# Performance work log

Measured on AMD Instinct MI355X. Metric: run time of the kernel, lower is better.

Reference implementation:

```python
import jax, jax.numpy as jnp
import numpy as np

EPS = 1e-5  # flax BatchNorm default epsilon


def setup_inputs() -> dict:
    key = jax.random.key(0)
    ks = jax.random.split(key, 4)
    E, D, H = 6400000, 12, 12
    N = 100000
    return {
        "edges": jax.random.normal(ks[0], (E, D), dtype=jnp.float32),
        "bn_scale": jnp.ones((D,), jnp.float32),
        "bn_bias": jnp.zeros((D,), jnp.float32),
        "bn_mean": jnp.zeros((D,), jnp.float32),
        "bn_var": jnp.ones((D,), jnp.float32),
        "W1": jax.random.normal(ks[1], (D, H), dtype=jnp.float32) / np.sqrt(D),
        "b1": jnp.zeros((H,), jnp.float32),
        "W2": jax.random.normal(ks[2], (H, H), dtype=jnp.float32) / np.sqrt(H),
        "b2": jnp.zeros((H,), jnp.float32),
        "receivers": jax.random.randint(ks[3], (E,), 0, N, dtype=jnp.int32),
        "num_nodes": N,
    }


def reference(edges, bn_scale, bn_bias, bn_mean, bn_var, W1, b1, W2, b2, receivers, num_nodes):
    # EdgeEncoder (eval mode): BatchNorm(running stats) -> Dense(12) -> ReLU -> Dense(12)
    x = (edges - bn_mean) * (bn_scale * jax.lax.rsqrt(bn_var + EPS)) + bn_bias
    x = jax.nn.relu(x @ W1 + b1)
    x = x @ W2 + b2  # [E, 12] per-edge messages
    # aggregate messages into receiver nodes (update_node_fn returns this directly)
    nodes = jax.ops.segment_sum(x, receivers, num_segments=num_nodes)  # [N, 12]
    return nodes
```

## Files before the change

### kernel.cpp

```cpp
#include <hip/hip_runtime.h>

#define D      12
#define ASTR   13
#define LOGNPB 7
#define NPB    128
#define CAPBF  5120
#define CAPF   9216
#define EPB    16384
#define ABLK   256
#define SBLK   256
#define CBLK   256
#define SPLIT  2

#define SWZ(p) ((p) ^ (((p) >> 5) & 31))

static __device__ __forceinline__ unsigned f2bf(float f) {
    union { float f; unsigned u; } v; v.f = f;
    unsigned r = v.u + 0x7FFFu + ((v.u >> 16) & 1u);
    return r >> 16;
}
static __device__ __forceinline__ float bf_lo(unsigned u) {
    union { unsigned u; float f; } v; v.u = u << 16; return v.f;
}
static __device__ __forceinline__ float bf_hi(unsigned u) {
    union { unsigned u; float f; } v; v.u = u & 0xFFFF0000u; return v.f;
}

__global__ __launch_bounds__(256) void cvt_bf16(
    const float* __restrict__ in, unsigned* __restrict__ outw,
    long n8 , long ntot )
{
    long i = (long)blockIdx.x * 256 + threadIdx.x;
    const long stride = (long)gridDim.x * 256;
    for (; i < n8; i += stride) {
        const float4* p = reinterpret_cast<const float4*>(in + i * 8);
        float4 a = p[0], b = p[1];
        uint4 w;
        w.x = f2bf(a.x) | (f2bf(a.y) << 16);
        w.y = f2bf(a.z) | (f2bf(a.w) << 16);
        w.z = f2bf(b.x) | (f2bf(b.y) << 16);
        w.w = f2bf(b.z) | (f2bf(b.w) << 16);
        reinterpret_cast<uint4*>(outw)[i] = w;
    }
    if (blockIdx.x == 0 && threadIdx.x == 0) {
        for (long j = n8 * 8; j < ntot; ++j)
            reinterpret_cast<unsigned short*>(outw)[j] = (unsigned short)f2bf(in[j]);
    }
}

__global__ __launch_bounds__(ABLK) void passA_hist(
    const int* __restrict__ receivers, long E, int nbuck,
    int* __restrict__ cnt )
{
    extern __shared__ int hist[];
    for (int i = threadIdx.x; i < nbuck; i += ABLK) hist[i] = 0;
    __syncthreads();
    long e0 = (long)blockIdx.x * EPB;
    long e1 = e0 + EPB; if (e1 > E) e1 = E;
    for (long e = e0 + threadIdx.x; e < e1; e += ABLK) {
        int r = receivers[e];
        atomicAdd(&hist[r >> LOGNPB], 1);
    }
    __syncthreads();
    int* row = cnt + (long)blockIdx.x * nbuck;
    for (int i = threadIdx.x; i < nbuck; i += ABLK) row[i] = hist[i];
}

__global__ __launch_bounds__(SBLK) void passS1_colscan(
    int* __restrict__ cnt, int nblk, int nbuck, int* __restrict__ totals)
{
    int b = blockIdx.x;
    int t = threadIdx.x;
    __shared__ int csum[SBLK];
    int per = (nblk + SBLK - 1) / SBLK;
    int i0 = t * per;
    int i1 = i0 + per; if (i1 > nblk) i1 = nblk;
    int s = 0;
    for (int i = i0; i < i1; ++i) s += cnt[(long)i * nbuck + b];
    csum[t] = s;
    __syncthreads();
    for (int off = 1; off < SBLK; off <<= 1) {
        int add = (t >= off) ? csum[t - off] : 0;
        __syncthreads();
        csum[t] += add;
        __syncthreads();
    }
    int run = csum[t] - s;
    for (int i = i0; i < i1; ++i) {
        long a = (long)i * nbuck + b;
        int tmp = cnt[a];
        cnt[a] = run;
        run += tmp;
    }
    if (t == SBLK - 1) totals[b] = csum[SBLK - 1];
}

__global__ __launch_bounds__(1024) void passS2_basescan(
    const int* __restrict__ totals, int* __restrict__ base, int nbuck)
{
    __shared__ int sh[1024];
    int t = threadIdx.x;
    int v = (t < nbuck) ? totals[t] : 0;
    sh[t] = v;
    __syncthreads();
    for (int off = 1; off < 1024; off <<= 1) {
        int add = (t >= off) ? sh[t - off] : 0;
        __syncthreads();
        sh[t] += add;
        __syncthreads();
    }
    if (t < nbuck) base[t] = sh[t] - v;
}

__global__ __launch_bounds__(ABLK) void passB_scatter(
    const int* __restrict__ receivers, long E, int nbuck,
    const int* __restrict__ cnt, const int* __restrict__ base,
    unsigned int* __restrict__ sorted)
{
    extern __shared__ int cur[];
    const int* row = cnt + (long)blockIdx.x * nbuck;
    for (int i = threadIdx.x; i < nbuck; i += ABLK) cur[i] = row[i] + base[i];
    __syncthreads();
    long e0 = (long)blockIdx.x * EPB;
    long e1 = e0 + EPB; if (e1 > E) e1 = E;
    for (long e = e0 + threadIdx.x; e < e1; e += ABLK) {
        int r = receivers[e];
        int b = r >> LOGNPB;
        int pos = atomicAdd(&cur[b], 1);
        sorted[pos] = ((unsigned)e << LOGNPB) | (unsigned)(r & (NPB - 1));
    }
}

__device__ __forceinline__ void build_weights(
    int t,
    const float* __restrict__ bn_scale, const float* __restrict__ bn_bias,
    const float* __restrict__ bn_mean,  const float* __restrict__ bn_var,
    const float* __restrict__ W1, const float* __restrict__ b1,
    const float* __restrict__ W2, const float* __restrict__ b2,
    float* sW1, float* sW2, float* sB1, float* sB2)
{
    if (t < D * D) {
        int d = t / D;
        float a = bn_scale[d] * rsqrtf(bn_var[d] + 1e-5f);
        sW1[t] = a * W1[t];
        sW2[t] = W2[t];
    }
    if (t < D) {
        float acc = b1[t];
        #pragma unroll
        for (int d = 0; d < D; ++d) {
            float a = bn_scale[d] * rsqrtf(bn_var[d] + 1e-5f);
            float c = bn_bias[d] - bn_mean[d] * a;
            acc += c * W1[d * D + t];
        }
        sB1[t] = acc;
        sB2[t] = b2[t];
    }
}

__device__ __forceinline__ void mlp12(
    const float x[D],
    const float* sW1, const float* sW2, const float* sB1, const float* sB2,
    float y[D])
{
    float h[D];
    #pragma unroll
    for (int j = 0; j < D; ++j) h[j] = sB1[j];
    #pragma unroll
    for (int d = 0; d < D; ++d) {
        float xd = x[d];
        #pragma unroll
        for (int j = 0; j < D; ++j) h[j] = fmaf(xd, sW1[d * D + j], h[j]);
    }
    #pragma unroll
    for (int j = 0; j < D; ++j) h[j] = fmaxf(h[j], 0.f);
    #pragma unroll
    for (int j = 0; j < D; ++j) y[j] = sB2[j];
    #pragma unroll
    for (int d = 0; d < D; ++d) {
        float hd = h[d];
        #pragma unroll
        for (int j = 0; j < D; ++j) y[j] = fmaf(hd, sW2[d * D + j], y[j]);
    }
}

__global__ __launch_bounds__(CBLK) void passC_bf(
    const uint2* __restrict__ bfrows,
    const unsigned int* __restrict__ sortedG,
    const int* __restrict__ base, const int* __restrict__ totals,
    const float* __restrict__ bn_scale, const float* __restrict__ bn_bias,
    const float* __restrict__ bn_mean,  const float* __restrict__ bn_var,
    const float* __restrict__ W1, const float* __restrict__ b1,
    const float* __restrict__ W2, const float* __restrict__ b2,
    float* __restrict__ part,
    float* __restrict__ out,
    long total , long slab )
{
    __shared__ float sW1[D * D], sW2[D * D], sB1[D], sB2[D];
    __shared__ int hist[NPB];
    __shared__ int off[NPB + 1];
    __shared__ int cur[NPB];
    __shared__ unsigned sorted2[CAPBF];
    __shared__ float facc[NPB * ASTR];

    const int t = threadIdx.x;
    build_weights(t, bn_scale, bn_bias, bn_mean, bn_var, W1, b1, W2, b2,
                  sW1, sW2, sB1, sB2);
    for (int i = t; i < NPB * ASTR; i += CBLK) facc[i] = 0.f;
    if (t < NPB) hist[t] = 0;
    __syncthreads();

    const int b = blockIdx.x;
    const int s = blockIdx.y;
    const int S = gridDim.y;
    const int s0 = base[b];
    const int n  = totals[b];
    const int chunk = (n + S - 1) / S;
    const int g0 = s * chunk;
    int g1 = g0 + chunk; if (g1 > n) g1 = n;
    const int ns = g1 - g0;
    const unsigned* __restrict__ src = sortedG + s0 + g0;

    if (ns > 0 && ns <= CAPBF) {
        for (int k = t; k < ns; k += CBLK)
            atomicAdd(&hist[src[k] & (NPB - 1)], 1);
        __syncthreads();

        int myh = (t < NPB) ? hist[t] : 0;
        if (t < NPB) off[t] = myh;
        __syncthreads();
        for (int d2 = 1; d2 < NPB; d2 <<= 1) {
            int add = 0;
            if (t < NPB && t >= d2) add = off[t - d2];
            __syncthreads();
            if (t < NPB) off[t] += add;
            __syncthreads();
        }
        if (t < NPB) cur[t] = off[t] - myh;
        __syncthreads();
        if (t < NPB) off[t] = cur[t];
        if (t == 0) off[NPB] = ns;
        __syncthreads();

        for (int k = t; k < ns; k += CBLK) {
            unsigned e = src[k];
            int pos = atomicAdd(&cur[e & (NPB - 1)], 1);
            sorted2[SWZ(pos)] = e >> LOGNPB;
        }
        __syncthreads();

        const int per = (ns + CBLK - 1) / CBLK;
        int k0 = t * per;
        int k1 = k0 + per; if (k1 > ns) k1 = ns;
        if (k0 < k1) {
            int cu = 0;
            while (off[cu + 1] <= k0) ++cu;
            int nodeEnd = off[cu + 1];

            float ac[D];
            #pragma unroll
            for (int j = 0; j < D; ++j) ac[j] = 0.f;

            const int kmax = k1 - 1;
            unsigned idx = sorted2[SWZ(k0)];
            const uint2* rp = bfrows + (size_t)idx * 3;
            uint2 r0 = rp[0], r1 = rp[1], r2 = rp[2];

            for (int k = k0; k < k1; ++k) {
                int kn = (k + 1 <= kmax) ? k + 1 : kmax;
                unsigned nidx = sorted2[SWZ(kn)];
                const uint2* q = bfrows + (size_t)nidx * 3;
                uint2 n0 = q[0], n1 = q[1], n2 = q[2];

                if (k >= nodeEnd) {
                    #pragma unroll
                    for (int j = 0; j < D; ++j) {
                        atomicAdd(&facc[cu * ASTR + j], ac[j]);
                        ac[j] = 0.f;
                    }
                    do { ++cu; } while (off[cu + 1] <= k);
                    nodeEnd = off[cu + 1];
                }

                float x[D] = {bf_lo(r0.x), bf_hi(r0.x), bf_lo(r0.y), bf_hi(r0.y),
                              bf_lo(r1.x), bf_hi(r1.x), bf_lo(r1.y), bf_hi(r1.y),
                              bf_lo(r2.x), bf_hi(r2.x), bf_lo(r2.y), bf_hi(r2.y)};
                float h[D];
                #pragma unroll
                for (int j = 0; j < D; ++j) h[j] = sB1[j];
                #pragma unroll
                for (int d = 0; d < D; ++d) {
                    float xd = x[d];
                    #pragma unroll
                    for (int j = 0; j < D; ++j) h[j] = fmaf(xd, sW1[d * D + j], h[j]);
                }
                #pragma unroll
                for (int j = 0; j < D; ++j) h[j] = fmaxf(h[j], 0.f);
                #pragma unroll
                for (int d = 0; d < D; ++d) {
                    float hd = h[d];
                    #pragma unroll
                    for (int j = 0; j < D; ++j) ac[j] = fmaf(hd, sW2[d * D + j], ac[j]);
                }
                r0 = n0; r1 = n1; r2 = n2;
            }
            #pragma unroll
            for (int j = 0; j < D; ++j) atomicAdd(&facc[cu * ASTR + j], ac[j]);
        }
    } else if (ns > 0) {
        for (int k = t; k < ns; k += CBLK) {
            unsigned e = src[k];
            const uint2* rp = bfrows + (size_t)(e >> LOGNPB) * 3;
            uint2 r0 = rp[0], r1 = rp[1], r2 = rp[2];
            float x[D] = {bf_lo(r0.x), bf_hi(r0.x), bf_lo(r0.y), bf_hi(r0.y),
                          bf_lo(r1.x), bf_hi(r1.x), bf_lo(r1.y), bf_hi(r1.y),
                          bf_lo(r2.x), bf_hi(r2.x), bf_lo(r2.y), bf_hi(r2.y)};
            float y[D];
            mlp12(x, sW1, sW2, sB1, sB2, y);
            int rloc = (int)(e & (NPB - 1));
            #pragma unroll
            for (int j = 0; j < D; ++j) atomicAdd(&facc[rloc * ASTR + j], y[j]);
        }
    }
    __syncthreads();

    if (part != nullptr) {
        float* dst = part + (long)s * slab + (long)b * (NPB * D);
        for (int i = t; i < NPB * D; i += CBLK) {
            int node = i / D, j = i % D;
            dst[i] = facc[node * ASTR + j] + (float)hist[node] * sB2[j];
        }
    } else {
        long obase = (long)b * (NPB * D);
        long cnt_w = total - obase; if (cnt_w > NPB * D) cnt_w = NPB * D;
        for (long i = t; i < cnt_w; i += CBLK) {
            int node = (int)i / D, j = (int)i % D;
            out[obase + i] = facc[node * ASTR + j] + (float)hist[node] * sB2[j];
        }
    }
}

__global__ __launch_bounds__(CBLK) void reduce_partials(
    const float* __restrict__ part, float* __restrict__ out,
    long total4, long slab4, int S)
{
    long i = (long)blockIdx.x * CBLK + threadIdx.x;
    if (i >= total4) return;
    const float4* p = reinterpret_cast<const float4*>(part);
    float4 v = p[i];
    for (int s = 1; s < S; ++s) {
        float4 w = p[(long)s * slab4 + i];
        v.x += w.x; v.y += w.y; v.z += w.z; v.w += w.w;
    }
    reinterpret_cast<float4*>(out)[i] = v;
}

__global__ __launch_bounds__(CBLK) void passC_f32(
    const float* __restrict__ edges,
    const unsigned int* __restrict__ sortedG,
    const int* __restrict__ base, const int* __restrict__ totals,
    const float* __restrict__ bn_scale, const float* __restrict__ bn_bias,
    const float* __restrict__ bn_mean,  const float* __restrict__ bn_var,
    const float* __restrict__ W1, const float* __restrict__ b1,
    const float* __restrict__ W2, const float* __restrict__ b2,
    float* __restrict__ out, long total)
{
    __shared__ float sW1[D * D], sW2[D * D], sB1[D], sB2[D];
    __shared__ int hist[NPB];
    __shared__ int off[NPB + 1];
    __shared__ int cur[NPB];
    __shared__ unsigned sorted2[CAPF];
    __shared__ float facc[NPB * ASTR];

    const int t = threadIdx.x;
    build_weights(t, bn_scale, bn_bias, bn_mean, bn_var, W1, b1, W2, b2,
                  sW1, sW2, sB1, sB2);
    for (int i = t; i < NPB * ASTR; i += CBLK) facc[i] = 0.f;
    if (t < NPB) hist[t] = 0;
    __syncthreads();

    const int b = blockIdx.x;
    const int s0 = base[b];
    const int n  = totals[b];

    if (n <= CAPF) {
        for (int k = t; k < n; k += CBLK)
            atomicAdd(&hist[sortedG[s0 + k] & (NPB - 1)], 1);
        __syncthreads();
        int myh = (t < NPB) ? hist[t] : 0;
        if (t < NPB) off[t] = myh;
        __syncthreads();
        for (int d2 = 1; d2 < NPB; d2 <<= 1) {
            int add = 0;
            if (t < NPB && t >= d2) add = off[t - d2];
            __syncthreads();
            if (t < NPB) off[t] += add;
            __syncthreads();
        }
        if (t < NPB) cur[t] = off[t] - myh;
        __syncthreads();
        if (t < NPB) off[t] = cur[t];
        if (t == 0) off[NPB] = n;
        __syncthreads();
        for (int k = t; k < n; k += CBLK) {
            unsigned e = sortedG[s0 + k];
            int pos = atomicAdd(&cur[e & (NPB - 1)], 1);
            sorted2[SWZ(pos)] = e >> LOGNPB;
        }
        __syncthreads();

        const int per = (n + CBLK - 1) / CBLK;
        int k0 = t * per;
        int k1 = k0 + per; if (k1 > n) k1 = n;
        if (k0 < k1) {
            int cu = 0;
            while (off[cu + 1] <= k0) ++cu;
            int nodeEnd = off[cu + 1];
            float ac[D];
            #pragma unroll
            for (int j = 0; j < D; ++j) ac[j] = 0.f;
            unsigned idx = sorted2[SWZ(k0)];
            const float4* p = reinterpret_cast<const float4*>(edges + (long)idx * D);
            float4 c0 = p[0], c1 = p[1], c2 = p[2];
            for (int k = k0; k < k1; ++k) {
                float4 n0 = c0, n1 = c1, n2 = c2;
                if (k + 1 < k1) {
                    unsigned ix = sorted2[SWZ(k + 1)];
                    const float4* q = reinterpret_cast<const float4*>(edges + (long)ix * D);
                    n0 = q[0]; n1 = q[1]; n2 = q[2];
                }
                if (k >= nodeEnd) {
                    #pragma unroll
                    for (int j = 0; j < D; ++j) {
                        atomicAdd(&facc[cu * ASTR + j], ac[j]);
                        ac[j] = 0.f;
                    }
                    do { ++cu; } while (off[cu + 1] <= k);
                    nodeEnd = off[cu + 1];
                }
                float x[D] = {c0.x, c0.y, c0.z, c0.w, c1.x, c1.y, c1.z, c1.w,
                              c2.x, c2.y, c2.z, c2.w};
                float y[D];
                mlp12(x, sW1, sW2, sB1, sB2, y);
                #pragma unroll
                for (int j = 0; j < D; ++j) ac[j] += y[j];
                c0 = n0; c1 = n1; c2 = n2;
            }
            #pragma unroll
            for (int j = 0; j < D; ++j) atomicAdd(&facc[cu * ASTR + j], ac[j]);
        }
    } else {
        for (int k = t; k < n; k += CBLK) {
            unsigned e = sortedG[s0 + k];
            const float4* p = reinterpret_cast<const float4*>(edges + (long)(e >> LOGNPB) * D);
            float4 c0 = p[0], c1 = p[1], c2 = p[2];
            float x[D] = {c0.x, c0.y, c0.z, c0.w, c1.x, c1.y, c1.z, c1.w,
                          c2.x, c2.y, c2.z, c2.w};
            float y[D];
            mlp12(x, sW1, sW2, sB1, sB2, y);
            int rloc = (int)(e & (NPB - 1));
            #pragma unroll
            for (int j = 0; j < D; ++j) atomicAdd(&facc[rloc * ASTR + j], y[j]);
        }
    }
    __syncthreads();

    long obase = (long)b * (NPB * D);
    long cnt_w = total - obase; if (cnt_w > NPB * D) cnt_w = NPB * D;
    for (long i = t; i < cnt_w; i += CBLK)
        out[obase + i] = facc[((int)i / D) * ASTR + ((int)i % D)];
}

#define EPT 4
__global__ __launch_bounds__(ABLK) void edge_mlp_scatter(
    const float* __restrict__ edges,
    const float* __restrict__ bn_scale, const float* __restrict__ bn_bias,
    const float* __restrict__ bn_mean,  const float* __restrict__ bn_var,
    const float* __restrict__ W1, const float* __restrict__ b1,
    const float* __restrict__ W2, const float* __restrict__ b2,
    const int* __restrict__ receivers, float* __restrict__ out, long E)
{
    __shared__ float sW1[D * D], sW2[D * D], sB1[D], sB2[D];
    const int t = threadIdx.x;
    build_weights(t, bn_scale, bn_bias, bn_mean, bn_var, W1, b1, W2, b2,
                  sW1, sW2, sB1, sB2);
    __syncthreads();
    const long basee = (long)blockIdx.x * (ABLK * EPT) + t;
    #pragma unroll
    for (int kk = 0; kk < EPT; ++kk) {
        long e = basee + (long)kk * ABLK;
        if (e >= E) continue;
        int r = receivers[e];
        const float4* p = reinterpret_cast<const float4*>(edges + e * D);
        float4 v0 = p[0], v1 = p[1], v2 = p[2];
        float x[D] = {v0.x, v0.y, v0.z, v0.w, v1.x, v1.y, v1.z, v1.w,
                      v2.x, v2.y, v2.z, v2.w};
        float y[D];
        mlp12(x, sW1, sW2, sB1, sB2, y);
        #pragma unroll
        for (int j = 0; j < D; ++j) atomicAdd(&out[(long)r * D + j], y[j]);
    }
}

extern "C" void kernel_launch(void* const* d_in, const int* in_sizes, int n_in,
                              void* d_out, int out_size, void* d_ws, size_t ws_size,
                              hipStream_t stream) {
    const float* edges     = (const float*)d_in[0];
    const float* bn_scale  = (const float*)d_in[1];
    const float* bn_bias   = (const float*)d_in[2];
    const float* bn_mean   = (const float*)d_in[3];
    const float* bn_var    = (const float*)d_in[4];
    const float* W1        = (const float*)d_in[5];
    const float* b1        = (const float*)d_in[6];
    const float* W2        = (const float*)d_in[7];
    const float* b2        = (const float*)d_in[8];
    const int*   receivers = (const int*)d_in[9];
    float*       out       = (float*)d_out;

    const long E = (long)in_sizes[0] / D;
    const int  N = out_size / D;

    const int  nbuck = (N + NPB - 1) >> LOGNPB;
    const long nblk  = (E + EPB - 1) / EPB;
    const size_t cntBytes  = (size_t)nblk * (size_t)nbuck * 4u;
    const size_t head      = cntBytes + 2u * (size_t)nbuck * 4u + 512u;
    const size_t bfBytes   = (size_t)E * 24u;
    const size_t slabBytes = (size_t)nbuck * (size_t)(NPB * D) * 4u;
    const size_t needT1 = head + (size_t)E * 4u + bfBytes + (size_t)SPLIT * slabBytes + 1024u;
    const size_t needT2 = head + (size_t)E * 4u;
    const long total = (long)N * D;

    const bool shapeOK = (nbuck <= 1024) && (E < (1L << 25));
    const size_t lds = (size_t)nbuck * 4u;

    if (shapeOK && ws_size >= needT1) {
        char* w = (char*)d_ws;
        int* cnt    = (int*)w;  w += cntBytes;
        int* totals = (int*)w;  w += (size_t)nbuck * 4u;
        int* basep  = (int*)w;  w += (size_t)nbuck * 4u;
        unsigned int* sortedG = (unsigned int*)w;  w += (size_t)E * 4u;
        unsigned* bfw = (unsigned*)(((uintptr_t)w + 255u) & ~(uintptr_t)255u);
        w = (char*)bfw + bfBytes;
        float* part = (float*)(((uintptr_t)w + 255u) & ~(uintptr_t)255u);

        const long ntot = E * D;
        const long n8 = ntot / 8;
        cvt_bf16      <<<dim3(2048), dim3(256), 0, stream>>>(edges, bfw, n8, ntot);
        passA_hist    <<<dim3((unsigned)nblk), dim3(ABLK), lds, stream>>>(receivers, E, nbuck, cnt);
        passS1_colscan<<<dim3((unsigned)nbuck), dim3(SBLK), 0, stream>>>(cnt, (int)nblk, nbuck, totals);
        passS2_basescan<<<dim3(1), dim3(1024), 0, stream>>>(totals, basep, nbuck);
        passB_scatter <<<dim3((unsigned)nblk), dim3(ABLK), lds, stream>>>(receivers, E, nbuck, cnt, basep, sortedG);

        const long slab = (long)nbuck * (NPB * D);
        passC_bf      <<<dim3((unsigned)nbuck, SPLIT), dim3(CBLK), 0, stream>>>(
            (const uint2*)bfw, sortedG, basep, totals,
            bn_scale, bn_bias, bn_mean, bn_var, W1, b1, W2, b2,
            part, out, total, slab);
        const long total4 = total / 4;
        const long rblocks = (total4 + CBLK - 1) / CBLK;
        reduce_partials<<<dim3((unsigned)rblocks), dim3(CBLK), 0, stream>>>(
            part, out, total4, slab / 4, SPLIT);
        return;
    }

    if (shapeOK && ws_size >= needT2) {
        char* w = (char*)d_ws;
        int* cnt    = (int*)w;  w += cntBytes;
        int* totals = (int*)w;  w += (size_t)nbuck * 4u;
        int* basep  = (int*)w;  w += (size_t)nbuck * 4u;
        unsigned int* sortedG = (unsigned int*)w;

        passA_hist    <<<dim3((unsigned)nblk), dim3(ABLK), lds, stream>>>(receivers, E, nbuck, cnt);
        passS1_colscan<<<dim3((unsigned)nbuck), dim3(SBLK), 0, stream>>>(cnt, (int)nblk, nbuck, totals);
        passS2_basescan<<<dim3(1), dim3(1024), 0, stream>>>(totals, basep, nbuck);
        passB_scatter <<<dim3((unsigned)nblk), dim3(ABLK), lds, stream>>>(receivers, E, nbuck, cnt, basep, sortedG);
        passC_f32     <<<dim3((unsigned)nbuck), dim3(CBLK), 0, stream>>>(
            edges, sortedG, basep, totals,
            bn_scale, bn_bias, bn_mean, bn_var, W1, b1, W2, b2, out, total);
        return;
    }

    (void)hipMemsetAsync(d_out, 0, (size_t)out_size * sizeof(float), stream);
    const long blocks = (E + (long)(ABLK * EPT) - 1) / (long)(ABLK * EPT);
    edge_mlp_scatter<<<dim3((unsigned)blocks), dim3(ABLK), 0, stream>>>(
        edges, bn_scale, bn_bias, bn_mean, bn_var, W1, b1, W2, b2,
        receivers, out, E);
}
```

Before: 427.4 us.

## Fuse bf16 conversion into histogram pass and process two edges per iteration

Drops the standalone fp32-to-bf16 conversion kernel and does the conversion inside the histogram pass, which saves one launch and lets the edge block partitioning be shared. EPB is halved, giving more histogram blocks and a larger count matrix for the column scan. The per-node accumulation loop in passC now handles two edges per iteration, with prefetches for two rows ahead, to raise ILP and memory-level parallelism at the cost of more registers and extra branching at node boundaries. The shape guard is also tightened.

```diff
diff --git a/kernel.cpp b/kernel.cpp
--- a/kernel.cpp
+++ b/kernel.cpp
@@ -6,7 +6,7 @@
 #define NPB    128
 #define CAPBF  5120
 #define CAPF   9216
-#define EPB    16384
+#define EPB    8192
 #define ABLK   256
 #define SBLK   256
 #define CBLK   256
@@ -25,41 +25,47 @@
 static __device__ __forceinline__ float bf_hi(unsigned u) {
     union { unsigned u; float f; } v; v.u = u & 0xFFFF0000u; return v.f;
 }
-
-__global__ __launch_bounds__(256) void cvt_bf16(
-    const float* __restrict__ in, unsigned* __restrict__ outw,
-    long n8 , long ntot )
-{
-    long i = (long)blockIdx.x * 256 + threadIdx.x;
-    const long stride = (long)gridDim.x * 256;
-    for (; i < n8; i += stride) {
-        const float4* p = reinterpret_cast<const float4*>(in + i * 8);
-        float4 a = p[0], b = p[1];
-        uint4 w;
-        w.x = f2bf(a.x) | (f2bf(a.y) << 16);
-        w.y = f2bf(a.z) | (f2bf(a.w) << 16);
-        w.z = f2bf(b.x) | (f2bf(b.y) << 16);
-        w.w = f2bf(b.z) | (f2bf(b.w) << 16);
-        reinterpret_cast<uint4*>(outw)[i] = w;
-    }
-    if (blockIdx.x == 0 && threadIdx.x == 0) {
-        for (long j = n8 * 8; j < ntot; ++j)
-            reinterpret_cast<unsigned short*>(outw)[j] = (unsigned short)f2bf(in[j]);
-    }
-}
-
-__global__ __launch_bounds__(ABLK) void passA_hist(
-    const int* __restrict__ receivers, long E, int nbuck,
-    int* __restrict__ cnt )
+static __device__ __forceinline__ unsigned pk(float a, float b) {
+    return f2bf(a) | (f2bf(b) << 16);
+}
+
+__global__ __launch_bounds__(ABLK) void passA_hist_cvt(
+    const int* __restrict__ receivers, const float* __restrict__ edges,
+    unsigned* __restrict__ bfw, long E, int nbuck, int* __restrict__ cnt)
 {
     extern __shared__ int hist[];
     for (int i = threadIdx.x; i < nbuck; i += ABLK) hist[i] = 0;
     __syncthreads();
-    long e0 = (long)blockIdx.x * EPB;
+    const long e0 = (long)blockIdx.x * EPB;
     long e1 = e0 + EPB; if (e1 > E) e1 = E;
+
     for (long e = e0 + threadIdx.x; e < e1; e += ABLK) {
         int r = receivers[e];
         atomicAdd(&hist[r >> LOGNPB], 1);
+    }
+
+    if (bfw != nullptr) {
+        for (long pe = e0 + 2L * threadIdx.x; pe < e1; pe += 2L * ABLK) {
+            const float4* p = reinterpret_cast<const float4*>(edges + pe * D);
+            float4 a0 = p[0], a1 = p[1], a2 = p[2];
+            if (pe + 1 < e1) {
+                float4 b0 = p[3], b1 = p[4], b2 = p[5];
+                uint4 w0, w1, w2;
+                w0.x = pk(a0.x, a0.y); w0.y = pk(a0.z, a0.w);
+                w0.z = pk(a1.x, a1.y); w0.w = pk(a1.z, a1.w);
+                w1.x = pk(a2.x, a2.y); w1.y = pk(a2.z, a2.w);
+                w1.z = pk(b0.x, b0.y); w1.w = pk(b0.z, b0.w);
+                w2.x = pk(b1.x, b1.y); w2.y = pk(b1.z, b1.w);
+                w2.z = pk(b2.x, b2.y); w2.w = pk(b2.z, b2.w);
+                uint4* dst = reinterpret_cast<uint4*>(bfw) + (pe >> 1) * 3;
+                dst[0] = w0; dst[1] = w1; dst[2] = w2;
+            } else {
+                uint2* dst = reinterpret_cast<uint2*>(bfw) + pe * 3;
+                dst[0] = make_uint2(pk(a0.x, a0.y), pk(a0.z, a0.w));
+                dst[1] = make_uint2(pk(a1.x, a1.y), pk(a1.z, a1.w));
+                dst[2] = make_uint2(pk(a2.x, a2.y), pk(a2.z, a2.w));
+            }
+        }
     }
     __syncthreads();
     int* row = cnt + (long)blockIdx.x * nbuck;
@@ -192,9 +198,8 @@
     const float* __restrict__ bn_mean,  const float* __restrict__ bn_var,
     const float* __restrict__ W1, const float* __restrict__ b1,
     const float* __restrict__ W2, const float* __restrict__ b2,
-    float* __restrict__ part,
-    float* __restrict__ out,
-    long total , long slab )
+    float* __restrict__ part, float* __restrict__ out,
+    long total, long slab)
 {
     __shared__ float sW1[D * D], sW2[D * D], sB1[D], sB2[D];
     __shared__ int hist[NPB];
@@ -262,15 +267,22 @@
             for (int j = 0; j < D; ++j) ac[j] = 0.f;
 
             const int kmax = k1 - 1;
-            unsigned idx = sorted2[SWZ(k0)];
-            const uint2* rp = bfrows + (size_t)idx * 3;
-            uint2 r0 = rp[0], r1 = rp[1], r2 = rp[2];
-
-            for (int k = k0; k < k1; ++k) {
-                int kn = (k + 1 <= kmax) ? k + 1 : kmax;
-                unsigned nidx = sorted2[SWZ(kn)];
-                const uint2* q = bfrows + (size_t)nidx * 3;
-                uint2 n0 = q[0], n1 = q[1], n2 = q[2];
+            unsigned iA = sorted2[SWZ(k0)];
+            unsigned iB = sorted2[SWZ((k0 + 1 <= kmax) ? k0 + 1 : kmax)];
+            const uint2* pA = bfrows + (size_t)iA * 3;
+            const uint2* pB = bfrows + (size_t)iB * 3;
+            uint2 a0 = pA[0], a1 = pA[1], a2 = pA[2];
+            uint2 c0 = pB[0], c1 = pB[1], c2 = pB[2];
+
+            for (int k = k0; k < k1; k += 2) {
+                int kn0 = (k + 2 <= kmax) ? k + 2 : kmax;
+                int kn1 = (k + 3 <= kmax) ? k + 3 : kmax;
+                unsigned jA = sorted2[SWZ(kn0)];
+                unsigned jB = sorted2[SWZ(kn1)];
+                const uint2* qA = bfrows + (size_t)jA * 3;
+                const uint2* qB = bfrows + (size_t)jB * 3;
+                uint2 na0 = qA[0], na1 = qA[1], na2 = qA[2];
+                uint2 nb0 = qB[0], nb1 = qB[1], nb2 = qB[2];
 
                 if (k >= nodeEnd) {
                     #pragma unroll
@@ -281,28 +293,95 @@
                     do { ++cu; } while (off[cu + 1] <= k);
                     nodeEnd = off[cu + 1];
                 }
-
-                float x[D] = {bf_lo(r0.x), bf_hi(r0.x), bf_lo(r0.y), bf_hi(r0.y),
-                              bf_lo(r1.x), bf_hi(r1.x), bf_lo(r1.y), bf_hi(r1.y),
-                              bf_lo(r2.x), bf_hi(r2.x), bf_lo(r2.y), bf_hi(r2.y)};
-                float h[D];
-                #pragma unroll
-                for (int j = 0; j < D; ++j) h[j] = sB1[j];
-                #pragma unroll
-                for (int d = 0; d < D; ++d) {
-                    float xd = x[d];
+                const bool hasB = (k + 1 < k1);
+                float x0[D] = {bf_lo(a0.x), bf_hi(a0.x), bf_lo(a0.y), bf_hi(a0.y),
+                               bf_lo(a1.x), bf_hi(a1.x), bf_lo(a1.y), bf_hi(a1.y),
+                               bf_lo(a2.x), bf_hi(a2.x), bf_lo(a2.y), bf_hi(a2.y)};
+                if (hasB && (k + 1 < nodeEnd)) {
+                    float x1[D] = {bf_lo(c0.x), bf_hi(c0.x), bf_lo(c0.y), bf_hi(c0.y),
+                                   bf_lo(c1.x), bf_hi(c1.x), bf_lo(c1.y), bf_hi(c1.y),
+                                   bf_lo(c2.x), bf_hi(c2.x), bf_lo(c2.y), bf_hi(c2.y)};
+                    float h0[D], h1[D];
                     #pragma unroll
-                    for (int j = 0; j < D; ++j) h[j] = fmaf(xd, sW1[d * D + j], h[j]);
+                    for (int j = 0; j < D; ++j) { float bj = sB1[j]; h0[j] = bj; h1[j] = bj; }
+                    #pragma unroll
+                    for (int d = 0; d < D; ++d) {
+                        float xa = x0[d], xb = x1[d];
+                        #pragma unroll
+                        for (int j = 0; j < D; ++j) {
+                            float w = sW1[d * D + j];
+                            h0[j] = fmaf(xa, w, h0[j]);
+                            h1[j] = fmaf(xb, w, h1[j]);
+                        }
+                    }
+                    #pragma unroll
+                    for (int j = 0; j < D; ++j) {
+                        h0[j] = fmaxf(h0[j], 0.f);
+                        h1[j] = fmaxf(h1[j], 0.f);
+                    }
+                    #pragma unroll
+                    for (int d = 0; d < D; ++d) {
+                        float ha = h0[d], hb = h1[d];
+                        #pragma unroll
+                        for (int j = 0; j < D; ++j) {
+                            float w = sW2[d * D + j];
+                            ac[j] = fmaf(ha, w, fmaf(hb, w, ac[j]));
+                        }
+                    }
+                } else {
+                    {
+                        float h[D];
+                        #pragma unroll
+                        for (int j = 0; j < D; ++j) h[j] = sB1[j];
+                        #pragma unroll
+                        for (int d = 0; d < D; ++d) {
+                            float xd = x0[d];
+                            #pragma unroll
+                            for (int j = 0; j < D; ++j) h[j] = fmaf(xd, sW1[d * D + j], h[j]);
+                        }
+                        #pragma unroll
+                        for (int j = 0; j < D; ++j) h[j] = fmaxf(h[j], 0.f);
+                        #pragma unroll
+                        for (int d = 0; d < D; ++d) {
+                            float hd = h[d];
+                            #pragma unroll
+                            for (int j = 0; j < D; ++j) ac[j] = fmaf(hd, sW2[d * D + j], ac[j]);
+                        }
+                    }
+                    if (hasB) {
+                        if (k + 1 >= nodeEnd) {
+                            #pragma unroll
+                            for (int j = 0; j < D; ++j) {
+                                atomicAdd(&facc[cu * ASTR + j], ac[j]);
+                                ac[j] = 0.f;
+                            }
+                            do { ++cu; } while (off[cu + 1] <= k + 1);
+                            nodeEnd = off[cu + 1];
+                        }
+                        float x1[D] = {bf_lo(c0.x), bf_hi(c0.x), bf_lo(c0.y), bf_hi(c0.y),
+                                       bf_lo(c1.x), bf_hi(c1.x), bf_lo(c1.y), bf_hi(c1.y),
+                                       bf_lo(c2.x), bf_hi(c2.x), bf_lo(c2.y), bf_hi(c2.y)};
+                        float h[D];
+                        #pragma unroll
+                        for (int j = 0; j < D; ++j) h[j] = sB1[j];
+                        #pragma unroll
+                        for (int d = 0; d < D; ++d) {
+                            float xd = x1[d];
+                            #pragma unroll
+                            for (int j = 0; j < D; ++j) h[j] = fmaf(xd, sW1[d * D + j], h[j]);
+                        }
+                        #pragma unroll
+                        for (int j = 0; j < D; ++j) h[j] = fmaxf(h[j], 0.f);
+                        #pragma unroll
+                        for (int d = 0; d < D; ++d) {
+                            float hd = h[d];
+                            #pragma unroll
+                            for (int j = 0; j < D; ++j) ac[j] = fmaf(hd, sW2[d * D + j], ac[j]);
+                        }
+                    }
                 }
-                #pragma unroll
-                for (int j = 0; j < D; ++j) h[j] = fmaxf(h[j], 0.f);
-                #pragma unroll
-                for (int d = 0; d < D; ++d) {
-                    float hd = h[d];
-                    #pragma unroll
-                    for (int j = 0; j < D; ++j) ac[j] = fmaf(hd, sW2[d * D + j], ac[j]);
-                }
-                r0 = n0; r1 = n1; r2 = n2;
+                a0 = na0; a1 = na1; a2 = na2;
+                c0 = nb0; c1 = nb1; c2 = nb2;
             }
             #pragma unroll
             for (int j = 0; j < D; ++j) atomicAdd(&facc[cu * ASTR + j], ac[j]);
@@ -530,7 +609,7 @@
     const size_t needT2 = head + (size_t)E * 4u;
     const long total = (long)N * D;
 
-    const bool shapeOK = (nbuck <= 1024) && (E < (1L << 25));
+    const bool shapeOK = (nbuck <= 1024) && (E < (1L << 24));
     const size_t lds = (size_t)nbuck * 4u;
 
     if (shapeOK && ws_size >= needT1) {
@@ -543,10 +622,8 @@
         w = (char*)bfw + bfBytes;
         float* part = (float*)(((uintptr_t)w + 255u) & ~(uintptr_t)255u);
 
-        const long ntot = E * D;
-        const long n8 = ntot / 8;
-        cvt_bf16      <<<dim3(2048), dim3(256), 0, stream>>>(edges, bfw, n8, ntot);
-        passA_hist    <<<dim3((unsigned)nblk), dim3(ABLK), lds, stream>>>(receivers, E, nbuck, cnt);
+        passA_hist_cvt<<<dim3((unsigned)nblk), dim3(ABLK), lds, stream>>>(
+            receivers, edges, bfw, E, nbuck, cnt);
         passS1_colscan<<<dim3((unsigned)nbuck), dim3(SBLK), 0, stream>>>(cnt, (int)nblk, nbuck, totals);
         passS2_basescan<<<dim3(1), dim3(1024), 0, stream>>>(totals, basep, nbuck);
         passB_scatter <<<dim3((unsigned)nblk), dim3(ABLK), lds, stream>>>(receivers, E, nbuck, cnt, basep, sortedG);
@@ -570,7 +647,8 @@
         int* basep  = (int*)w;  w += (size_t)nbuck * 4u;
         unsigned int* sortedG = (unsigned int*)w;
 
-        passA_hist    <<<dim3((unsigned)nblk), dim3(ABLK), lds, stream>>>(receivers, E, nbuck, cnt);
+        passA_hist_cvt<<<dim3((unsigned)nblk), dim3(ABLK), lds, stream>>>(
+            receivers, edges, nullptr, E, nbuck, cnt);
         passS1_colscan<<<dim3((unsigned)nbuck), dim3(SBLK), 0, stream>>>(cnt, (int)nblk, nbuck, totals);
         passS2_basescan<<<dim3(1), dim3(1024), 0, stream>>>(totals, basep, nbuck);
         passB_scatter <<<dim3((unsigned)nblk), dim3(ABLK), lds, stream>>>(receivers, E, nbuck, cnt, basep, sortedG);
```

Measured after the change: 662.6 us. 55.0% more time.

## Compute per-edge MLP in histogram pass, store bf16 messages, sum-only gather

Applied to the files above, without the earlier changes.

Moves the BN+MLP computation out of the sorted gather kernel into the coalesced histogram pass, which now reads fp32 edges directly and writes bf16 per-edge messages. This removes the separate bf16 conversion kernel and makes the gather kernel a plain bf16 sum with a deeper two-ahead prefetch. Block sizes change as well (EPB halved, SPLIT doubled, a smaller LDS sort capacity). The trade-off is that messages rather than inputs are rounded to bf16, and the E limit is tightened to 2^24 because EPB is smaller.

```diff
diff --git a/kernel.cpp b/kernel.cpp
--- a/kernel.cpp
+++ b/kernel.cpp
@@ -4,13 +4,13 @@
 #define ASTR   13
 #define LOGNPB 7
 #define NPB    128
-#define CAPBF  5120
+#define CAPS   2944
 #define CAPF   9216
-#define EPB    16384
+#define EPB    8192
 #define ABLK   256
 #define SBLK   256
 #define CBLK   256
-#define SPLIT  2
+#define SPLIT  4
 
 #define SWZ(p) ((p) ^ (((p) >> 5) & 31))
 
@@ -25,32 +25,107 @@
 static __device__ __forceinline__ float bf_hi(unsigned u) {
     union { unsigned u; float f; } v; v.u = u & 0xFFFF0000u; return v.f;
 }
-
-__global__ __launch_bounds__(256) void cvt_bf16(
-    const float* __restrict__ in, unsigned* __restrict__ outw,
-    long n8 , long ntot )
-{
-    long i = (long)blockIdx.x * 256 + threadIdx.x;
-    const long stride = (long)gridDim.x * 256;
-    for (; i < n8; i += stride) {
-        const float4* p = reinterpret_cast<const float4*>(in + i * 8);
-        float4 a = p[0], b = p[1];
-        uint4 w;
-        w.x = f2bf(a.x) | (f2bf(a.y) << 16);
-        w.y = f2bf(a.z) | (f2bf(a.w) << 16);
-        w.z = f2bf(b.x) | (f2bf(b.y) << 16);
-        w.w = f2bf(b.z) | (f2bf(b.w) << 16);
-        reinterpret_cast<uint4*>(outw)[i] = w;
-    }
-    if (blockIdx.x == 0 && threadIdx.x == 0) {
-        for (long j = n8 * 8; j < ntot; ++j)
-            reinterpret_cast<unsigned short*>(outw)[j] = (unsigned short)f2bf(in[j]);
-    }
+static __device__ __forceinline__ unsigned pk(float a, float b) {
+    return f2bf(a) | (f2bf(b) << 16);
+}
+
+__device__ __forceinline__ void build_weights(
+    int t,
+    const float* __restrict__ bn_scale, const float* __restrict__ bn_bias,
+    const float* __restrict__ bn_mean,  const float* __restrict__ bn_var,
+    const float* __restrict__ W1, const float* __restrict__ b1,
+    const float* __restrict__ W2, const float* __restrict__ b2,
+    float* sW1, float* sW2, float* sB1, float* sB2)
+{
+    if (t < D * D) {
+        int d = t / D;
+        float a = bn_scale[d] * rsqrtf(bn_var[d] + 1e-5f);
+        sW1[t] = a * W1[t];
+        sW2[t] = W2[t];
+    }
+    if (t < D) {
+        float acc = b1[t];
+        #pragma unroll
+        for (int d = 0; d < D; ++d) {
+            float a = bn_scale[d] * rsqrtf(bn_var[d] + 1e-5f);
+            float c = bn_bias[d] - bn_mean[d] * a;
+            acc += c * W1[d * D + t];
+        }
+        sB1[t] = acc;
+        sB2[t] = b2[t];
+    }
+}
+
+__device__ __forceinline__ void mlp12(
+    const float x[D],
+    const float* sW1, const float* sW2, const float* sB1, const float* sB2,
+    float y[D])
+{
+    float h[D];
+    #pragma unroll
+    for (int j = 0; j < D; ++j) h[j] = sB1[j];
+    #pragma unroll
+    for (int d = 0; d < D; ++d) {
+        float xd = x[d];
+        #pragma unroll
+        for (int j = 0; j < D; ++j) h[j] = fmaf(xd, sW1[d * D + j], h[j]);
+    }
+    #pragma unroll
+    for (int j = 0; j < D; ++j) h[j] = fmaxf(h[j], 0.f);
+    #pragma unroll
+    for (int j = 0; j < D; ++j) y[j] = sB2[j];
+    #pragma unroll
+    for (int d = 0; d < D; ++d) {
+        float hd = h[d];
+        #pragma unroll
+        for (int j = 0; j < D; ++j) y[j] = fmaf(hd, sW2[d * D + j], y[j]);
+    }
+}
+
+__global__ __launch_bounds__(ABLK) void passA_cvt_mlp(
+    const int* __restrict__ receivers, const float* __restrict__ edges,
+    unsigned* __restrict__ msg ,
+    long E, int nbuck, int* __restrict__ cnt,
+    const float* __restrict__ bn_scale, const float* __restrict__ bn_bias,
+    const float* __restrict__ bn_mean,  const float* __restrict__ bn_var,
+    const float* __restrict__ W1, const float* __restrict__ b1,
+    const float* __restrict__ W2, const float* __restrict__ b2)
+{
+    __shared__ float sW1[D * D], sW2[D * D], sB1[D], sB2[D];
+    extern __shared__ int hist[];
+    const int t = threadIdx.x;
+    for (int i = t; i < nbuck; i += ABLK) hist[i] = 0;
+    build_weights(t, bn_scale, bn_bias, bn_mean, bn_var, W1, b1, W2, b2,
+                  sW1, sW2, sB1, sB2);
+    __syncthreads();
+
+    const long e0 = (long)blockIdx.x * EPB;
+    long e1 = e0 + EPB; if (e1 > E) e1 = E;
+
+    for (long e = e0 + t; e < e1; e += ABLK) {
+        int r = receivers[e];
+        atomicAdd(&hist[r >> LOGNPB], 1);
+
+        const float4* p = reinterpret_cast<const float4*>(edges + e * D);
+        float4 v0 = p[0], v1 = p[1], v2 = p[2];
+        float x[D] = {v0.x, v0.y, v0.z, v0.w, v1.x, v1.y, v1.z, v1.w,
+                      v2.x, v2.y, v2.z, v2.w};
+        float y[D];
+        mlp12(x, sW1, sW2, sB1, sB2, y);
+
+        uint2* dst = reinterpret_cast<uint2*>(msg + (size_t)e * 6u);
+        dst[0] = make_uint2(pk(y[0], y[1]),  pk(y[2], y[3]));
+        dst[1] = make_uint2(pk(y[4], y[5]),  pk(y[6], y[7]));
+        dst[2] = make_uint2(pk(y[8], y[9]),  pk(y[10], y[11]));
+    }
+    __syncthreads();
+    int* row = cnt + (long)blockIdx.x * nbuck;
+    for (int i = t; i < nbuck; i += ABLK) row[i] = hist[i];
 }
 
 __global__ __launch_bounds__(ABLK) void passA_hist(
     const int* __restrict__ receivers, long E, int nbuck,
-    int* __restrict__ cnt )
+    int* __restrict__ cnt)
 {
     extern __shared__ int hist[];
     for (int i = threadIdx.x; i < nbuck; i += ABLK) hist[i] = 0;
@@ -131,81 +206,21 @@
     }
 }
 
-__device__ __forceinline__ void build_weights(
-    int t,
-    const float* __restrict__ bn_scale, const float* __restrict__ bn_bias,
-    const float* __restrict__ bn_mean,  const float* __restrict__ bn_var,
-    const float* __restrict__ W1, const float* __restrict__ b1,
-    const float* __restrict__ W2, const float* __restrict__ b2,
-    float* sW1, float* sW2, float* sB1, float* sB2)
-{
-    if (t < D * D) {
-        int d = t / D;
-        float a = bn_scale[d] * rsqrtf(bn_var[d] + 1e-5f);
-        sW1[t] = a * W1[t];
-        sW2[t] = W2[t];
-    }
-    if (t < D) {
-        float acc = b1[t];
-        #pragma unroll
-        for (int d = 0; d < D; ++d) {
-            float a = bn_scale[d] * rsqrtf(bn_var[d] + 1e-5f);
-            float c = bn_bias[d] - bn_mean[d] * a;
-            acc += c * W1[d * D + t];
-        }
-        sB1[t] = acc;
-        sB2[t] = b2[t];
-    }
-}
-
-__device__ __forceinline__ void mlp12(
-    const float x[D],
-    const float* sW1, const float* sW2, const float* sB1, const float* sB2,
-    float y[D])
-{
-    float h[D];
-    #pragma unroll
-    for (int j = 0; j < D; ++j) h[j] = sB1[j];
-    #pragma unroll
-    for (int d = 0; d < D; ++d) {
-        float xd = x[d];
-        #pragma unroll
-        for (int j = 0; j < D; ++j) h[j] = fmaf(xd, sW1[d * D + j], h[j]);
-    }
-    #pragma unroll
-    for (int j = 0; j < D; ++j) h[j] = fmaxf(h[j], 0.f);
-    #pragma unroll
-    for (int j = 0; j < D; ++j) y[j] = sB2[j];
-    #pragma unroll
-    for (int d = 0; d < D; ++d) {
-        float hd = h[d];
-        #pragma unroll
-        for (int j = 0; j < D; ++j) y[j] = fmaf(hd, sW2[d * D + j], y[j]);
-    }
-}
-
-__global__ __launch_bounds__(CBLK) void passC_bf(
-    const uint2* __restrict__ bfrows,
+__global__ __launch_bounds__(CBLK) void passC_sum(
+    const unsigned* __restrict__ msg,
     const unsigned int* __restrict__ sortedG,
     const int* __restrict__ base, const int* __restrict__ totals,
-    const float* __restrict__ bn_scale, const float* __restrict__ bn_bias,
-    const float* __restrict__ bn_mean,  const float* __restrict__ bn_var,
-    const float* __restrict__ W1, const float* __restrict__ b1,
-    const float* __restrict__ W2, const float* __restrict__ b2,
     float* __restrict__ part,
     float* __restrict__ out,
     long total , long slab )
 {
-    __shared__ float sW1[D * D], sW2[D * D], sB1[D], sB2[D];
     __shared__ int hist[NPB];
     __shared__ int off[NPB + 1];
     __shared__ int cur[NPB];
-    __shared__ unsigned sorted2[CAPBF];
+    __shared__ unsigned sorted2[CAPS];
     __shared__ float facc[NPB * ASTR];
 
     const int t = threadIdx.x;
-    build_weights(t, bn_scale, bn_bias, bn_mean, bn_var, W1, b1, W2, b2,
-                  sW1, sW2, sB1, sB2);
     for (int i = t; i < NPB * ASTR; i += CBLK) facc[i] = 0.f;
     if (t < NPB) hist[t] = 0;
     __syncthreads();
@@ -221,7 +236,7 @@
     const int ns = g1 - g0;
     const unsigned* __restrict__ src = sortedG + s0 + g0;
 
-    if (ns > 0 && ns <= CAPBF) {
+    if (ns > 0 && ns <= CAPS) {
         for (int k = t; k < ns; k += CBLK)
             atomicAdd(&hist[src[k] & (NPB - 1)], 1);
         __syncthreads();
@@ -262,15 +277,18 @@
             for (int j = 0; j < D; ++j) ac[j] = 0.f;
 
             const int kmax = k1 - 1;
-            unsigned idx = sorted2[SWZ(k0)];
-            const uint2* rp = bfrows + (size_t)idx * 3;
-            uint2 r0 = rp[0], r1 = rp[1], r2 = rp[2];
+            unsigned iA = sorted2[SWZ(k0)];
+            unsigned iB = sorted2[SWZ((k0 + 1 <= kmax) ? k0 + 1 : kmax)];
+            const uint2* pA = reinterpret_cast<const uint2*>(msg + (size_t)iA * 6u);
+            const uint2* pB = reinterpret_cast<const uint2*>(msg + (size_t)iB * 6u);
+            uint2 a0 = pA[0], a1 = pA[1], a2 = pA[2];
+            uint2 b0 = pB[0], b1 = pB[1], b2 = pB[2];
 
             for (int k = k0; k < k1; ++k) {
-                int kn = (k + 1 <= kmax) ? k + 1 : kmax;
-                unsigned nidx = sorted2[SWZ(kn)];
-                const uint2* q = bfrows + (size_t)nidx * 3;
-                uint2 n0 = q[0], n1 = q[1], n2 = q[2];
+                int kc = (k + 2 <= kmax) ? k + 2 : kmax;
+                unsigned iC = sorted2[SWZ(kc)];
+                const uint2* pC = reinterpret_cast<const uint2*>(msg + (size_t)iC * 6u);
+                uint2 c0 = pC[0], c1 = pC[1], c2 = pC[2];
 
                 if (k >= nodeEnd) {
                     #pragma unroll
@@ -281,28 +299,15 @@
                     do { ++cu; } while (off[cu + 1] <= k);
                     nodeEnd = off[cu + 1];
                 }
-
-                float x[D] = {bf_lo(r0.x), bf_hi(r0.x), bf_lo(r0.y), bf_hi(r0.y),
-                              bf_lo(r1.x), bf_hi(r1.x), bf_lo(r1.y), bf_hi(r1.y),
-                              bf_lo(r2.x), bf_hi(r2.x), bf_lo(r2.y), bf_hi(r2.y)};
-                float h[D];
-                #pragma unroll
-                for (int j = 0; j < D; ++j) h[j] = sB1[j];
-                #pragma unroll
-                for (int d = 0; d < D; ++d) {
-                    float xd = x[d];
-                    #pragma unroll
-                    for (int j = 0; j < D; ++j) h[j] = fmaf(xd, sW1[d * D + j], h[j]);
-                }
-                #pragma unroll
-                for (int j = 0; j < D; ++j) h[j] = fmaxf(h[j], 0.f);
-                #pragma unroll
-                for (int d = 0; d < D; ++d) {
-                    float hd = h[d];
-                    #pragma unroll
-                    for (int j = 0; j < D; ++j) ac[j] = fmaf(hd, sW2[d * D + j], ac[j]);
-                }
-                r0 = n0; r1 = n1; r2 = n2;
+                ac[0]  += bf_lo(a0.x); ac[1]  += bf_hi(a0.x);
+                ac[2]  += bf_lo(a0.y); ac[3]  += bf_hi(a0.y);
+                ac[4]  += bf_lo(a1.x); ac[5]  += bf_hi(a1.x);
+                ac[6]  += bf_lo(a1.y); ac[7]  += bf_hi(a1.y);
+                ac[8]  += bf_lo(a2.x); ac[9]  += bf_hi(a2.x);
+                ac[10] += bf_lo(a2.y); ac[11] += bf_hi(a2.y);
+
+                a0 = b0; a1 = b1; a2 = b2;
+                b0 = c0; b1 = c1; b2 = c2;
             }
             #pragma unroll
             for (int j = 0; j < D; ++j) atomicAdd(&facc[cu * ASTR + j], ac[j]);
@@ -310,33 +315,34 @@
     } else if (ns > 0) {
         for (int k = t; k < ns; k += CBLK) {
             unsigned e = src[k];
-            const uint2* rp = bfrows + (size_t)(e >> LOGNPB) * 3;
+            const uint2* rp = reinterpret_cast<const uint2*>(msg + (size_t)(e >> LOGNPB) * 6u);
             uint2 r0 = rp[0], r1 = rp[1], r2 = rp[2];
-            float x[D] = {bf_lo(r0.x), bf_hi(r0.x), bf_lo(r0.y), bf_hi(r0.y),
-                          bf_lo(r1.x), bf_hi(r1.x), bf_lo(r1.y), bf_hi(r1.y),
-                          bf_lo(r2.x), bf_hi(r2.x), bf_lo(r2.y), bf_hi(r2.y)};
-            float y[D];
-            mlp12(x, sW1, sW2, sB1, sB2, y);
-            int rloc = (int)(e & (NPB - 1));
-            #pragma unroll
-            for (int j = 0; j < D; ++j) atomicAdd(&facc[rloc * ASTR + j], y[j]);
+            int rl = (int)(e & (NPB - 1));
+            atomicAdd(&facc[rl * ASTR + 0],  bf_lo(r0.x));
+            atomicAdd(&facc[rl * ASTR + 1],  bf_hi(r0.x));
+            atomicAdd(&facc[rl * ASTR + 2],  bf_lo(r0.y));
+            atomicAdd(&facc[rl * ASTR + 3],  bf_hi(r0.y));
+            atomicAdd(&facc[rl * ASTR + 4],  bf_lo(r1.x));
+            atomicAdd(&facc[rl * ASTR + 5],  bf_hi(r1.x));
+            atomicAdd(&facc[rl * ASTR + 6],  bf_lo(r1.y));
+            atomicAdd(&facc[rl * ASTR + 7],  bf_hi(r1.y));
+            atomicAdd(&facc[rl * ASTR + 8],  bf_lo(r2.x));
+            atomicAdd(&facc[rl * ASTR + 9],  bf_hi(r2.x));
+            atomicAdd(&facc[rl * ASTR + 10], bf_lo(r2.y));
+            atomicAdd(&facc[rl * ASTR + 11], bf_hi(r2.y));
         }
     }
     __syncthreads();
 
     if (part != nullptr) {
         float* dst = part + (long)s * slab + (long)b * (NPB * D);
-        for (int i = t; i < NPB * D; i += CBLK) {
-            int node = i / D, j = i % D;
-            dst[i] = facc[node * ASTR + j] + (float)hist[node] * sB2[j];
-        }
+        for (int i = t; i < NPB * D; i += CBLK)
+            dst[i] = facc[(i / D) * ASTR + (i % D)];
     } else {
         long obase = (long)b * (NPB * D);
         long cnt_w = total - obase; if (cnt_w > NPB * D) cnt_w = NPB * D;
-        for (long i = t; i < cnt_w; i += CBLK) {
-            int node = (int)i / D, j = (int)i % D;
-            out[obase + i] = facc[node * ASTR + j] + (float)hist[node] * sB2[j];
-        }
+        for (long i = t; i < cnt_w; i += CBLK)
+            out[obase + i] = facc[((int)i / D) * ASTR + ((int)i % D)];
     }
 }
 
@@ -524,13 +530,13 @@
     const long nblk  = (E + EPB - 1) / EPB;
     const size_t cntBytes  = (size_t)nblk * (size_t)nbuck * 4u;
     const size_t head      = cntBytes + 2u * (size_t)nbuck * 4u + 512u;
-    const size_t bfBytes   = (size_t)E * 24u;
+    const size_t msgBytes  = (size_t)E * 24u;
     const size_t slabBytes = (size_t)nbuck * (size_t)(NPB * D) * 4u;
-    const size_t needT1 = head + (size_t)E * 4u + bfBytes + (size_t)SPLIT * slabBytes + 1024u;
+    const size_t needT1 = head + (size_t)E * 4u + msgBytes + (size_t)SPLIT * slabBytes + 1024u;
     const size_t needT2 = head + (size_t)E * 4u;
     const long total = (long)N * D;
 
-    const bool shapeOK = (nbuck <= 1024) && (E < (1L << 25));
+    const bool shapeOK = (nbuck <= 1024) && (E < (1L << 24));
     const size_t lds = (size_t)nbuck * 4u;
 
     if (shapeOK && ws_size >= needT1) {
@@ -539,23 +545,20 @@
         int* totals = (int*)w;  w += (size_t)nbuck * 4u;
         int* basep  = (int*)w;  w += (size_t)nbuck * 4u;
         unsigned int* sortedG = (unsigned int*)w;  w += (size_t)E * 4u;
-        unsigned* bfw = (unsigned*)(((uintptr_t)w + 255u) & ~(uintptr_t)255u);
-        w = (char*)bfw + bfBytes;
+        unsigned* msg = (unsigned*)(((uintptr_t)w + 255u) & ~(uintptr_t)255u);
+        w = (char*)msg + msgBytes;
         float* part = (float*)(((uintptr_t)w + 255u) & ~(uintptr_t)255u);
 
-        const long ntot = E * D;
-        const long n8 = ntot / 8;
-        cvt_bf16      <<<dim3(2048), dim3(256), 0, stream>>>(edges, bfw, n8, ntot);
-        passA_hist    <<<dim3((unsigned)nblk), dim3(ABLK), lds, stream>>>(receivers, E, nbuck, cnt);
+        passA_cvt_mlp <<<dim3((unsigned)nblk), dim3(ABLK), lds, stream>>>(
+            receivers, edges, msg, E, nbuck, cnt,
+            bn_scale, bn_bias, bn_mean, bn_var, W1, b1, W2, b2);
         passS1_colscan<<<dim3((unsigned)nbuck), dim3(SBLK), 0, stream>>>(cnt, (int)nblk, nbuck, totals);
         passS2_basescan<<<dim3(1), dim3(1024), 0, stream>>>(totals, basep, nbuck);
         passB_scatter <<<dim3((unsigned)nblk), dim3(ABLK), lds, stream>>>(receivers, E, nbuck, cnt, basep, sortedG);
 
         const long slab = (long)nbuck * (NPB * D);
-        passC_bf      <<<dim3((unsigned)nbuck, SPLIT), dim3(CBLK), 0, stream>>>(
-            (const uint2*)bfw, sortedG, basep, totals,
-            bn_scale, bn_bias, bn_mean, bn_var, W1, b1, W2, b2,
-            part, out, total, slab);
+        passC_sum     <<<dim3((unsigned)nbuck, SPLIT), dim3(CBLK), 0, stream>>>(
+            msg, sortedG, basep, totals, part, out, total, slab);
         const long total4 = total / 4;
         const long rblocks = (total4 + CBLK - 1) / CBLK;
         reduce_partials<<<dim3((unsigned)rblocks), dim3(CBLK), 0, stream>>>(
```

Result: slower. 550.7 us (+28.8%).
